# Kernel optimization log

Hardware: AMD Instinct MI355X
Metric: run time of the kernel (lower is better)

The kernel has to match this reference:

```python
import jax, jax.numpy as jnp
import numpy as np

B = 32768
IN_DIM, OUT_DIM, VAR_DIM = 2, 3, 50
KER_DIMS = [1024, 1024, 1024, 1024]
NSTEPS = 32  # fixed-step RK4 stand-in for adaptive odeint over t in [0, 1]


def setup_inputs() -> dict:
    key = jax.random.key(0)
    ks = jax.random.split(key, 11)
    x = jax.random.normal(ks[0], (B, IN_DIM), dtype=jnp.float32)
    dims = [VAR_DIM] + KER_DIMS + [VAR_DIM]
    inp = {"x": x}
    for i, (d1, d2) in enumerate(zip(dims[:-1], dims[1:])):
        # torch Linear(d1+1, d2): weight (d2, d1+1); stored here as (d1+1, d2)
        bound = 1.0 / np.sqrt(d1 + 1)
        inp[f"W{i}"] = jax.random.uniform(ks[1 + 2 * i], (d1 + 1, d2), jnp.float32, -bound, bound)
        inp[f"b{i}"] = jax.random.uniform(ks[2 + 2 * i], (d2,), jnp.float32, -bound, bound)
    return inp


def _odefunc(t, y, Ws, bs):
    # Each layer: concat time column, Linear, ReLU (except last) -- matches ODEfunc.forward
    out = y
    n = len(Ws)
    for i in range(n):
        tcol = jnp.full((out.shape[0], 1), t, dtype=out.dtype)
        h = jnp.concatenate([out, tcol], axis=1)
        out = h @ Ws[i] + bs[i]
        if i < n - 1:
            out = jax.nn.relu(out)
    return out


def _integrate(x, Ws, bs):
    # Pad input into var_dim state: out[:, :in_dim] = x, rest zeros
    y0 = jnp.zeros((x.shape[0], VAR_DIM), dtype=x.dtype).at[:, : x.shape[1]].set(x)
    dt = jnp.asarray(1.0 / NSTEPS, dtype=x.dtype)
    ts = jnp.arange(NSTEPS, dtype=x.dtype) * dt

    def step(y, t):
        k1 = _odefunc(t, y, Ws, bs)
        k2 = _odefunc(t + dt * 0.5, y + dt * 0.5 * k1, Ws, bs)
        k3 = _odefunc(t + dt * 0.5, y + dt * 0.5 * k2, Ws, bs)
        k4 = _odefunc(t + dt, y + dt * k3, Ws, bs)
        return y + (dt / 6.0) * (k1 + 2.0 * k2 + 2.0 * k3 + k4), None

    y1, _ = jax.lax.scan(step, y0, ts)
    return y1[:, :OUT_DIM]


def reference(x, W0, b0, W1, b1, W2, b2, W3, b3, W4, b4):
    Ws = (W0, W1, W2, W3, W4)
    bs = (b0, b1, b2, b3, b4)
    return _integrate(x, Ws, bs)
```

## Files before the change

### kernel.cpp

```cpp
#include <hip/hip_runtime.h>
#include <hip/hip_bf16.h>
#include <stdint.h>


typedef __bf16 bf16_t;
typedef bf16_t bf16x8 __attribute__((ext_vector_type(8)));
typedef float  f32x4  __attribute__((ext_vector_type(4)));

#define DEVI static __device__ __forceinline__

DEVI void gload_lds16(const bf16_t* gsrc, bf16_t* ldst) {
  __builtin_amdgcn_global_load_lds(
      (const __attribute__((address_space(1))) uint32_t*)gsrc,
      (__attribute__((address_space(3))) uint32_t*)ldst,
      16, 0, 0);
}

template<int K>
__global__ __launch_bounds__(512, 2) void gemm256(
    const bf16_t* __restrict__ A,
    const bf16_t* __restrict__ BT,
    const float* __restrict__ bias,
    const float* __restrict__ wtime,
    float t,
    bf16_t* __restrict__ C, int ldc,
    int M, int N)
{
  constexpr int NT = K / 64;
  static_assert(NT >= 2, "need >=2 K-tiles");

  __shared__ __align__(16) bf16_t As[2][256][64];
  __shared__ __align__(16) bf16_t Bs[2][256][64];

  const int tid  = threadIdx.x;
  const int wave = tid >> 6;
  const int lane = tid & 63;
  const int wr = wave >> 2;
  const int wc = wave & 3;

  int wg = blockIdx.x;
  {
    const int cpx = gridDim.x >> 3;
    wg = (wg & 7) * cpx + (wg >> 3);
  }
  const int nbn = N >> 8;
  const int bm = (wg / nbn) << 8;
  const int bn = (wg % nbn) << 8;

  const int srow = lane >> 3;
  const int scol = ((lane & 7) << 3) ^ ((lane & 32) >> 1) ^ ((wave & 1) << 5);
  const bf16_t* aS = A  + (size_t)(bm + wave * 8 + srow) * K + scol;
  const bf16_t* bS = BT + (size_t)(bn + wave * 8 + srow) * K + scol;
  bf16_t* aD = &As[0][0][0] + wave * 8 * 64;
  bf16_t* bD = &Bs[0][0][0] + wave * 8 * 64;

  auto stageHalf = [&](int kt, int isB, int h) {
    const int buf = kt & 1;
    const bf16_t* src = (isB ? bS : aS) + (size_t)(h * 128) * K + kt * 64;
    bf16_t*       dst = (isB ? bD : aD) + (buf * 256 + h * 128) * 64;
    gload_lds16(src,                  dst);
    gload_lds16(src + (size_t)64 * K, dst + 64 * 64);
  };
  auto stageTile = [&](int kt) {
    stageHalf(kt, 0, 0); stageHalf(kt, 0, 1);
    stageHalf(kt, 1, 0); stageHalf(kt, 1, 1);
  };

  const int fr = lane & 15;
  const int fq = lane >> 4;
  const int rsw = ((fr & 4) << 3) ^ ((fr & 8) << 3);

  bf16x8 ah0[8], ah1[8];
  bf16x8 bh0[4], bh1[4];
  f32x4  acc[8][4] = {};

  auto lda_into = [&](bf16x8 (&dst)[8], int buf, int mh) {
    const char* base = (const char*)&As[buf][0][0];
#pragma unroll
    for (int m = 0; m < 4; ++m)
#pragma unroll
      for (int kk = 0; kk < 2; ++kk) {
        int r  = wr * 128 + (mh * 4 + m) * 16 + fr;
        int cb = (kk * 64 + fq * 16) ^ rsw;
        dst[m * 2 + kk] = *(const bf16x8*)(base + r * 128 + cb);
      }
  };
  auto ldb_into = [&](bf16x8 (&dst)[4], int buf, int nh) {
    const char* base = (const char*)&Bs[buf][0][0];
#pragma unroll
    for (int n = 0; n < 2; ++n)
#pragma unroll
      for (int kk = 0; kk < 2; ++kk) {
        int r  = wc * 64 + (nh * 2 + n) * 16 + fr;
        int cb = (kk * 64 + fq * 16) ^ rsw;
        dst[n * 2 + kk] = *(const bf16x8*)(base + r * 128 + cb);
      }
  };
  auto mma_quad = [&](bf16x8 (&a)[8], bf16x8 (&b)[4], int mh, int nh) {
    __builtin_amdgcn_s_setprio(1);
#pragma unroll
    for (int m = 0; m < 4; ++m)
#pragma unroll
      for (int n = 0; n < 2; ++n)
#pragma unroll
        for (int kk = 0; kk < 2; ++kk)
          acc[mh * 4 + m][nh * 2 + n] = __builtin_amdgcn_mfma_f32_16x16x32_bf16(
              a[m * 2 + kk], b[n * 2 + kk],
              acc[mh * 4 + m][nh * 2 + n], 0, 0, 0);
    __builtin_amdgcn_s_setprio(0);
  };

  stageTile(0);
  asm volatile("s_waitcnt vmcnt(0)" ::: "memory");
  __builtin_amdgcn_s_barrier();
  lda_into(ah0, 0, 0);
  ldb_into(bh0, 0, 0);

  for (int t2 = 0; t2 < NT; ++t2) {
    const int buf = t2 & 1;
    if (t2 + 1 < NT) stageTile(t2 + 1);
    ldb_into(bh1, buf, 1);
    mma_quad(ah0, bh0, 0, 0);
    lda_into(ah1, buf, 1);
    mma_quad(ah0, bh1, 0, 1);
    mma_quad(ah1, bh0, 1, 0);
    if (t2 + 1 < NT) {
      asm volatile("s_waitcnt vmcnt(0)" ::: "memory");
      __builtin_amdgcn_s_barrier();
      lda_into(ah0, buf ^ 1, 0);
      ldb_into(bh0, buf ^ 1, 0);
    }
    mma_quad(ah1, bh1, 1, 1);
  }

#pragma unroll
  for (int n = 0; n < 4; ++n) {
    const int gcol = bn + wc * 64 + n * 16 + fr;
    const float bv = bias[gcol] + t * wtime[gcol];
#pragma unroll
    for (int m = 0; m < 8; ++m) {
      const int grow0 = bm + wr * 128 + m * 16 + (fq << 2);
#pragma unroll
      for (int r = 0; r < 4; ++r) {
        float v = acc[m][n][r] + bv;
        v = v > 0.0f ? v : 0.0f;
        C[(size_t)(grow0 + r) * ldc + gcol] = (bf16_t)v;
      }
    }
  }
}

template<int BM, int BN, int BK, int WROWS, int WCOLS, bool RELU, bool OUT_BF16>
__global__ __launch_bounds__(256) void gemm_bt(
    const bf16_t* __restrict__ A, int lda,
    const bf16_t* __restrict__ BT,
    const float* __restrict__ bias,
    const float* __restrict__ wtime,
    float t,
    void* __restrict__ Cv, int ldc,
    int M, int K)
{
  static_assert(BK == 64, "swizzle assumes BK=64");
  constexpr int MR  = BM / WROWS / 16;
  constexpr int NR  = BN / WCOLS / 16;
  constexpr int TPR = BK / 8;
  constexpr int RPW = 64 / TPR;
  constexpr int RPL = 4 * RPW;
  static_assert(BM % RPL == 0 && BN % RPL == 0, "tile staging mismatch");

  __shared__ bf16_t As[BM][BK];
  __shared__ bf16_t Bs[BN][BK];

  const int tid  = threadIdx.x;
  const int wave = tid >> 6;
  const int lane = tid & 63;
  const int wr = wave / WCOLS;
  const int wc = wave % WCOLS;
  const int bm = blockIdx.x * BM;
  const int bn = blockIdx.y * BN;
  const int lrow = lane >> 3;
  const int lcol = (((lane & 7) << 3) ^ ((lane & 32) >> 1) ^ ((wave & 1) << 5));

  const int fr = lane & 15;
  const int fq = lane >> 4;
  const int esw = ((fr & 4) << 2) ^ ((fr & 8) << 2);

  f32x4 acc[MR][NR] = {};

  for (int k0 = 0; k0 < K; k0 += BK) {
#pragma unroll
    for (int i = 0; i < BM / RPL; ++i) {
      const int rb = i * RPL + wave * RPW;
      gload_lds16(&A[(size_t)(bm + rb + lrow) * lda + k0 + lcol], &As[rb][0]);
    }
#pragma unroll
    for (int i = 0; i < BN / RPL; ++i) {
      const int rb = i * RPL + wave * RPW;
      gload_lds16(&BT[(size_t)(bn + rb + lrow) * K + k0 + lcol], &Bs[rb][0]);
    }
    __syncthreads();
#pragma unroll
    for (int kk = 0; kk < BK / 32; ++kk) {
      bf16x8 af[MR], bfr[NR];
      const int ecol = (kk * 32 + fq * 8) ^ esw;
#pragma unroll
      for (int m = 0; m < MR; ++m)
        af[m] = *(const bf16x8*)&As[wr * (BM / WROWS) + m * 16 + fr][ecol];
#pragma unroll
      for (int n = 0; n < NR; ++n)
        bfr[n] = *(const bf16x8*)&Bs[wc * (BN / WCOLS) + n * 16 + fr][ecol];
#pragma unroll
      for (int m = 0; m < MR; ++m)
#pragma unroll
        for (int n = 0; n < NR; ++n)
          acc[m][n] = __builtin_amdgcn_mfma_f32_16x16x32_bf16(
              af[m], bfr[n], acc[m][n], 0, 0, 0);
    }
    __syncthreads();
  }

#pragma unroll
  for (int n = 0; n < NR; ++n) {
    const int gcol = bn + wc * (BN / WCOLS) + n * 16 + fr;
    const float bv = bias[gcol] + t * wtime[gcol];
#pragma unroll
    for (int m = 0; m < MR; ++m) {
      const int grow0 = bm + wr * (BM / WROWS) + m * 16 + (fq << 2);
#pragma unroll
      for (int r = 0; r < 4; ++r) {
        float v = acc[m][n][r] + bv;
        if (RELU) v = v > 0.0f ? v : 0.0f;
        if constexpr (OUT_BF16)
          ((bf16_t*)Cv)[(size_t)(grow0 + r) * ldc + gcol] = (bf16_t)v;
        else
          ((float*)Cv)[(size_t)(grow0 + r) * ldc + gcol] = v;
      }
    }
  }
}

__global__ __launch_bounds__(256) void gemm_l4_rk4(
    const bf16_t* __restrict__ A, int lda,
    const bf16_t* __restrict__ BT,
    const float* __restrict__ bias,
    const float* __restrict__ wtime,
    float t,
    float* __restrict__ y, float* __restrict__ accb,
    bf16_t* __restrict__ ybf,
    float ca, float cs, int mode,
    int M, int K)
{
  constexpr int BM = 64, BN = 64, BK = 64;
  constexpr int MR = 2, NR = 2;

  __shared__ bf16_t As[BM][BK];
  __shared__ bf16_t Bs[BN][BK];

  const int tid  = threadIdx.x;
  const int wave = tid >> 6;
  const int lane = tid & 63;
  const int wr = wave >> 1;
  const int wc = wave & 1;
  const int bm = blockIdx.x * BM;
  const int lrow = lane >> 3;
  const int lcol = (((lane & 7) << 3) ^ ((lane & 32) >> 1) ^ ((wave & 1) << 5));

  const int fr = lane & 15;
  const int fq = lane >> 4;
  const int esw = ((fr & 4) << 2) ^ ((fr & 8) << 2);

  f32x4 acc[MR][NR] = {};

  for (int k0 = 0; k0 < K; k0 += BK) {
#pragma unroll
    for (int i = 0; i < 2; ++i) {
      const int rb = i * 32 + wave * 8;
      gload_lds16(&A[(size_t)(bm + rb + lrow) * lda + k0 + lcol], &As[rb][0]);
    }
#pragma unroll
    for (int i = 0; i < 2; ++i) {
      const int rb = i * 32 + wave * 8;
      gload_lds16(&BT[(size_t)(rb + lrow) * K + k0 + lcol], &Bs[rb][0]);
    }
    __syncthreads();
#pragma unroll
    for (int kk = 0; kk < 2; ++kk) {
      bf16x8 af[MR], bfr[NR];
      const int ecol = (kk * 32 + fq * 8) ^ esw;
#pragma unroll
      for (int m = 0; m < MR; ++m)
        af[m] = *(const bf16x8*)&As[wr * 32 + m * 16 + fr][ecol];
#pragma unroll
      for (int n = 0; n < NR; ++n)
        bfr[n] = *(const bf16x8*)&Bs[wc * 32 + n * 16 + fr][ecol];
#pragma unroll
      for (int m = 0; m < MR; ++m)
#pragma unroll
        for (int n = 0; n < NR; ++n)
          acc[m][n] = __builtin_amdgcn_mfma_f32_16x16x32_bf16(
              af[m], bfr[n], acc[m][n], 0, 0, 0);
    }
    __syncthreads();
  }

#pragma unroll
  for (int n = 0; n < NR; ++n) {
    const int gcol = wc * 32 + n * 16 + fr;
    const float bv = bias[gcol] + t * wtime[gcol];
#pragma unroll
    for (int m = 0; m < MR; ++m) {
      const int grow0 = bm + wr * 32 + m * 16 + (fq << 2);
#pragma unroll
      for (int r = 0; r < 4; ++r) {
        const float kv = acc[m][n][r] + bv;
        const size_t o = (size_t)(grow0 + r) * 64 + gcol;
        if (mode == 0) {
          accb[o] = kv;
          ybf[o] = (bf16_t)(y[o] + cs * kv);
        } else if (mode == 1) {
          accb[o] += ca * kv;
          ybf[o] = (bf16_t)(y[o] + cs * kv);
        } else {
          const float ny = y[o] + cs * (accb[o] + kv);
          y[o] = ny;
          ybf[o] = (bf16_t)ny;
        }
      }
    }
  }
}

__global__ void prep_weight(const float* __restrict__ W, const float* __restrict__ b,
                            bf16_t* __restrict__ WT, float* __restrict__ bias,
                            float* __restrict__ wtime,
                            int K, int N, int Kpad, int Npad)
{
  int idx = blockIdx.x * 256 + threadIdx.x;
  int total = Npad * Kpad;
  if (idx < total) {
    int n = idx / Kpad, k = idx % Kpad;
    float v = (n < N && k < K) ? W[(size_t)k * N + n] : 0.0f;
    WT[idx] = (bf16_t)v;
  }
  if (idx < Npad) {
    bias[idx]  = (idx < N) ? b[idx] : 0.0f;
    wtime[idx] = (idx < N) ? W[(size_t)K * N + idx] : 0.0f;
  }
}

__global__ void init_y(const float* __restrict__ x, float* __restrict__ y,
                       bf16_t* __restrict__ ybf, int M)
{
  int i = blockIdx.x * 256 + threadIdx.x;
  if (i < M * 64) {
    int m = i >> 6, c = i & 63;
    float v = (c < 2) ? x[m * 2 + c] : 0.0f;
    y[i] = v;
    ybf[i] = (bf16_t)v;
  }
}

__global__ void extract_out(const float* __restrict__ y, float* __restrict__ out, int M)
{
  int i = blockIdx.x * 256 + threadIdx.x;
  if (i < M * 3) {
    int m = i / 3, c = i % 3;
    out[i] = y[(size_t)m * 64 + c];
  }
}

extern "C" void kernel_launch(void* const* d_in, const int* in_sizes, int n_in,
                              void* d_out, int out_size, void* d_ws, size_t ws_size,
                              hipStream_t stream)
{
  (void)in_sizes; (void)n_in; (void)out_size; (void)ws_size;
  const int M = 32768;

  const float* x = (const float*)d_in[0];
  const float* Wp[5]; const float* bp[5];
  for (int i = 0; i < 5; ++i) {
    Wp[i] = (const float*)d_in[1 + 2 * i];
    bp[i] = (const float*)d_in[2 + 2 * i];
  }

  char* ws = (char*)d_ws; size_t off = 0;
  auto alloc = [&](size_t bytes) -> char* {
    char* p = ws + off; off += (bytes + 255) & ~(size_t)255; return p;
  };

  bf16_t* WT[5];
  WT[0] = (bf16_t*)alloc((size_t)1024 * 64 * 2);
  WT[1] = (bf16_t*)alloc((size_t)1024 * 1024 * 2);
  WT[2] = (bf16_t*)alloc((size_t)1024 * 1024 * 2);
  WT[3] = (bf16_t*)alloc((size_t)1024 * 1024 * 2);
  WT[4] = (bf16_t*)alloc((size_t)64 * 1024 * 2);
  float* bias[5]; float* wtm[5];
  for (int i = 0; i < 5; ++i) {
    int Np = (i == 4) ? 64 : 1024;
    bias[i] = (float*)alloc((size_t)Np * 4);
    wtm[i]  = (float*)alloc((size_t)Np * 4);
  }
  float*  y    = (float*)alloc((size_t)M * 64 * 4);
  float*  accb = (float*)alloc((size_t)M * 64 * 4);
  bf16_t* ybf  = (bf16_t*)alloc((size_t)M * 64 * 2);
  bf16_t* act0 = (bf16_t*)alloc((size_t)M * 1024 * 2);
  bf16_t* act1 = (bf16_t*)alloc((size_t)M * 1024 * 2);

  const int Kd[5]  = {50, 1024, 1024, 1024, 1024};
  const int Nd[5]  = {1024, 1024, 1024, 1024, 50};
  const int Kpd[5] = {64, 1024, 1024, 1024, 1024};
  const int Npd[5] = {1024, 1024, 1024, 1024, 64};
  for (int i = 0; i < 5; ++i) {
    int tot = Npd[i] * Kpd[i];
    prep_weight<<<dim3((tot + 255) / 256), 256, 0, stream>>>(
        Wp[i], bp[i], WT[i], bias[i], wtm[i], Kd[i], Nd[i], Kpd[i], Npd[i]);
  }

  init_y<<<dim3((M * 64 + 255) / 256), 256, 0, stream>>>(x, y, ybf, M);

  const float dtv = 1.0f / 32.0f;
  dim3 gL0(M / 128, 1024 / 128);
  dim3 g256(M / 256 * (1024 / 256));
  dim3 gL4(M / 64);

  auto run_net = [&](float t, float ca, float cs, int mode) {
    gemm_bt<128,128,64,2,2,true,true><<<gL0, 256, 0, stream>>>(
        ybf, 64, WT[0], bias[0], wtm[0], t, act0, 1024, M, 64);
    gemm256<1024><<<g256, 512, 0, stream>>>(
        act0, WT[1], bias[1], wtm[1], t, act1, 1024, M, 1024);
    gemm256<1024><<<g256, 512, 0, stream>>>(
        act1, WT[2], bias[2], wtm[2], t, act0, 1024, M, 1024);
    gemm256<1024><<<g256, 512, 0, stream>>>(
        act0, WT[3], bias[3], wtm[3], t, act1, 1024, M, 1024);
    gemm_l4_rk4<<<gL4, 256, 0, stream>>>(
        act1, 1024, WT[4], bias[4], wtm[4], t,
        y, accb, ybf, ca, cs, mode, M, 1024);
  };

  for (int i = 0; i < 32; ++i) {
    const float t0 = i * dtv;
    const float tm = t0 + 0.5f * dtv;
    const float t1 = t0 + dtv;
    run_net(t0, 0.0f, 0.5f * dtv, 0);
    run_net(tm, 2.0f, 0.5f * dtv, 1);
    run_net(tm, 2.0f, dtv,        1);
    run_net(t1, 0.0f, dtv / 6.0f, 2);
  }

  extract_out<<<dim3((M * 3 + 255) / 256), 256, 0, stream>>>(y, (float*)d_out, M);
}
```

Measured before the change: 35.17 ms.

## Use 4-wave 256x256 GEMM blocks with 128x128 per-wave tiles

The 1024x1024 hidden-layer GEMM kernel moves from 8 waves (2x4, 128x64 per wave) to 4 waves (2x2, 128x128 per wave) per 256x256 block. Each wave now holds 64 accumulator tiles, loads full 8-fragment A/B sets per k-substep and stages 16 LDS loads per tile. The aim is more MFMA work per LDS fragment read and fewer waves contending for LDS bandwidth. The cost is much higher register pressure and occupancy limited to one block per CU, which reduces latency hiding and risks spills.

```diff
diff --git a/kernel.cpp b/kernel.cpp
--- a/kernel.cpp
+++ b/kernel.cpp
@@ -17,7 +17,7 @@
 }
 
 template<int K>
-__global__ __launch_bounds__(512, 2) void gemm256(
+__global__ __launch_bounds__(256, 1) void gemm256(
     const bf16_t* __restrict__ A,
     const bf16_t* __restrict__ BT,
     const float* __restrict__ bias,
@@ -35,8 +35,8 @@
   const int tid  = threadIdx.x;
   const int wave = tid >> 6;
   const int lane = tid & 63;
-  const int wr = wave >> 2;
-  const int wc = wave & 3;
+  const int wr = wave >> 1;
+  const int wc = wave & 1;
 
   int wg = blockIdx.x;
   {
@@ -54,88 +54,77 @@
   bf16_t* aD = &As[0][0][0] + wave * 8 * 64;
   bf16_t* bD = &Bs[0][0][0] + wave * 8 * 64;
 
-  auto stageHalf = [&](int kt, int isB, int h) {
+  auto stageTile = [&](int kt) {
     const int buf = kt & 1;
-    const bf16_t* src = (isB ? bS : aS) + (size_t)(h * 128) * K + kt * 64;
-    bf16_t*       dst = (isB ? bD : aD) + (buf * 256 + h * 128) * 64;
-    gload_lds16(src,                  dst);
-    gload_lds16(src + (size_t)64 * K, dst + 64 * 64);
-  };
-  auto stageTile = [&](int kt) {
-    stageHalf(kt, 0, 0); stageHalf(kt, 0, 1);
-    stageHalf(kt, 1, 0); stageHalf(kt, 1, 1);
+#pragma unroll
+    for (int i = 0; i < 8; ++i) {
+      gload_lds16(aS + (size_t)(i * 32) * K + kt * 64, aD + (buf * 256 + i * 32) * 64);
+      gload_lds16(bS + (size_t)(i * 32) * K + kt * 64, bD + (buf * 256 + i * 32) * 64);
+    }
   };
 
   const int fr = lane & 15;
   const int fq = lane >> 4;
   const int rsw = ((fr & 4) << 3) ^ ((fr & 8) << 3);
 
-  bf16x8 ah0[8], ah1[8];
-  bf16x8 bh0[4], bh1[4];
-  f32x4  acc[8][4] = {};
-
-  auto lda_into = [&](bf16x8 (&dst)[8], int buf, int mh) {
+  bf16x8 a0[8], a1[8];
+  bf16x8 b0[8], b1[8];
+  f32x4  acc[8][8] = {};
+
+  auto lda_kk = [&](bf16x8 (&dst)[8], int buf, int kk) {
     const char* base = (const char*)&As[buf][0][0];
 #pragma unroll
-    for (int m = 0; m < 4; ++m)
-#pragma unroll
-      for (int kk = 0; kk < 2; ++kk) {
-        int r  = wr * 128 + (mh * 4 + m) * 16 + fr;
-        int cb = (kk * 64 + fq * 16) ^ rsw;
-        dst[m * 2 + kk] = *(const bf16x8*)(base + r * 128 + cb);
-      }
-  };
-  auto ldb_into = [&](bf16x8 (&dst)[4], int buf, int nh) {
+    for (int m = 0; m < 8; ++m) {
+      int r  = wr * 128 + m * 16 + fr;
+      int cb = (kk * 64 + fq * 16) ^ rsw;
+      dst[m] = *(const bf16x8*)(base + r * 128 + cb);
+    }
+  };
+  auto ldb_kk = [&](bf16x8 (&dst)[8], int buf, int kk) {
     const char* base = (const char*)&Bs[buf][0][0];
 #pragma unroll
-    for (int n = 0; n < 2; ++n)
-#pragma unroll
-      for (int kk = 0; kk < 2; ++kk) {
-        int r  = wc * 64 + (nh * 2 + n) * 16 + fr;
-        int cb = (kk * 64 + fq * 16) ^ rsw;
-        dst[n * 2 + kk] = *(const bf16x8*)(base + r * 128 + cb);
-      }
-  };
-  auto mma_quad = [&](bf16x8 (&a)[8], bf16x8 (&b)[4], int mh, int nh) {
+    for (int n = 0; n < 8; ++n) {
+      int r  = wc * 128 + n * 16 + fr;
+      int cb = (kk * 64 + fq * 16) ^ rsw;
+      dst[n] = *(const bf16x8*)(base + r * 128 + cb);
+    }
+  };
+  auto mma_all = [&](bf16x8 (&a)[8], bf16x8 (&b)[8]) {
     __builtin_amdgcn_s_setprio(1);
 #pragma unroll
-    for (int m = 0; m < 4; ++m)
-#pragma unroll
-      for (int n = 0; n < 2; ++n)
-#pragma unroll
-        for (int kk = 0; kk < 2; ++kk)
-          acc[mh * 4 + m][nh * 2 + n] = __builtin_amdgcn_mfma_f32_16x16x32_bf16(
-              a[m * 2 + kk], b[n * 2 + kk],
-              acc[mh * 4 + m][nh * 2 + n], 0, 0, 0);
+    for (int m = 0; m < 8; ++m)
+#pragma unroll
+      for (int n = 0; n < 8; ++n)
+        acc[m][n] = __builtin_amdgcn_mfma_f32_16x16x32_bf16(
+            a[m], b[n], acc[m][n], 0, 0, 0);
     __builtin_amdgcn_s_setprio(0);
   };
 
   stageTile(0);
   asm volatile("s_waitcnt vmcnt(0)" ::: "memory");
   __builtin_amdgcn_s_barrier();
-  lda_into(ah0, 0, 0);
-  ldb_into(bh0, 0, 0);
+  lda_kk(a0, 0, 0);
+  ldb_kk(b0, 0, 0);
 
   for (int t2 = 0; t2 < NT; ++t2) {
     const int buf = t2 & 1;
     if (t2 + 1 < NT) stageTile(t2 + 1);
-    ldb_into(bh1, buf, 1);
-    mma_quad(ah0, bh0, 0, 0);
-    lda_into(ah1, buf, 1);
-    mma_quad(ah0, bh1, 0, 1);
-    mma_quad(ah1, bh0, 1, 0);
+    lda_kk(a1, buf, 1);
+    ldb_kk(b1, buf, 1);
+    mma_all(a0, b0);
     if (t2 + 1 < NT) {
+      asm volatile("s_waitcnt lgkmcnt(0)" ::: "memory");
       asm volatile("s_waitcnt vmcnt(0)" ::: "memory");
       __builtin_amdgcn_s_barrier();
-      lda_into(ah0, buf ^ 1, 0);
-      ldb_into(bh0, buf ^ 1, 0);
-    }
-    mma_quad(ah1, bh1, 1, 1);
-  }
-
-#pragma unroll
-  for (int n = 0; n < 4; ++n) {
-    const int gcol = bn + wc * 64 + n * 16 + fr;
+      lda_kk(a0, buf ^ 1, 0);
+      ldb_kk(b0, buf ^ 1, 0);
+    }
+    mma_all(a1, b1);
+  }
+
+#pragma unroll
+  for (int n = 0; n < 8; ++n) {
+    const int gcol = bn + wc * 128 + n * 16 + fr;
     const float bv = bias[gcol] + t * wtime[gcol];
 #pragma unroll
     for (int m = 0; m < 8; ++m) {
@@ -426,11 +415,11 @@
   auto run_net = [&](float t, float ca, float cs, int mode) {
     gemm_bt<128,128,64,2,2,true,true><<<gL0, 256, 0, stream>>>(
         ybf, 64, WT[0], bias[0], wtm[0], t, act0, 1024, M, 64);
-    gemm256<1024><<<g256, 512, 0, stream>>>(
+    gemm256<1024><<<g256, 256, 0, stream>>>(
         act0, WT[1], bias[1], wtm[1], t, act1, 1024, M, 1024);
-    gemm256<1024><<<g256, 512, 0, stream>>>(
+    gemm256<1024><<<g256, 256, 0, stream>>>(
         act1, WT[2], bias[2], wtm[2], t, act0, 1024, M, 1024);
-    gemm256<1024><<<g256, 512, 0, stream>>>(
+    gemm256<1024><<<g256, 256, 0, stream>>>(
         act0, WT[3], bias[3], wtm[3], t, act1, 1024, M, 1024);
     gemm_l4_rk4<<<gL4, 256, 0, stream>>>(
         act1, 1024, WT[4], bias[4], wtm[4], t,
```

Measured after the change: 38.50 ms. 1.09x slower.

## Load B fragments directly from global into registers, drop B LDS staging

Applied to the files above, without the earlier changes.

B-operand tiles are no longer staged through shared memory. Each wave now reads its B fragments straight from global memory into registers, and the vmcnt waits are adjusted to overlap these loads with the MFMAs. This halves LDS use and removes the LDS writes and reads for B, which could allow more occupancy and less LDS traffic. In exchange, B rows are loaded redundantly across waves with less coalesced global accesses. The vmcnt counting is delicate: bh1 is loaded after the last mma, and the ordering of the waits relative to the A staging must be correct.

```diff
diff --git a/kernel.cpp b/kernel.cpp
--- a/kernel.cpp
+++ b/kernel.cpp
@@ -27,10 +27,9 @@
     int M, int N)
 {
   constexpr int NT = K / 64;
-  static_assert(NT >= 2, "need >=2 K-tiles");
+  static_assert(NT >= 3, "pipeline needs >=3 K-tiles");
 
   __shared__ __align__(16) bf16_t As[2][256][64];
-  __shared__ __align__(16) bf16_t Bs[2][256][64];
 
   const int tid  = threadIdx.x;
   const int wave = tid >> 6;
@@ -49,21 +48,18 @@
 
   const int srow = lane >> 3;
   const int scol = ((lane & 7) << 3) ^ ((lane & 32) >> 1) ^ ((wave & 1) << 5);
-  const bf16_t* aS = A  + (size_t)(bm + wave * 8 + srow) * K + scol;
-  const bf16_t* bS = BT + (size_t)(bn + wave * 8 + srow) * K + scol;
+  const bf16_t* aS = A + (size_t)(bm + wave * 8 + srow) * K + scol;
   bf16_t* aD = &As[0][0][0] + wave * 8 * 64;
-  bf16_t* bD = &Bs[0][0][0] + wave * 8 * 64;
-
-  auto stageHalf = [&](int kt, int isB, int h) {
+
+  auto stageTile = [&](int kt) {
     const int buf = kt & 1;
-    const bf16_t* src = (isB ? bS : aS) + (size_t)(h * 128) * K + kt * 64;
-    bf16_t*       dst = (isB ? bD : aD) + (buf * 256 + h * 128) * 64;
-    gload_lds16(src,                  dst);
-    gload_lds16(src + (size_t)64 * K, dst + 64 * 64);
-  };
-  auto stageTile = [&](int kt) {
-    stageHalf(kt, 0, 0); stageHalf(kt, 0, 1);
-    stageHalf(kt, 1, 0); stageHalf(kt, 1, 1);
+#pragma unroll
+    for (int h = 0; h < 2; ++h) {
+      const bf16_t* src = aS + (size_t)(h * 128) * K + kt * 64;
+      bf16_t*       dst = aD + (buf * 256 + h * 128) * 64;
+      gload_lds16(src,                  dst);
+      gload_lds16(src + (size_t)64 * K, dst + 64 * 64);
+    }
   };
 
   const int fr = lane & 15;
@@ -85,15 +81,14 @@
         dst[m * 2 + kk] = *(const bf16x8*)(base + r * 128 + cb);
       }
   };
-  auto ldb_into = [&](bf16x8 (&dst)[4], int buf, int nh) {
-    const char* base = (const char*)&Bs[buf][0][0];
+  auto ldbg = [&](bf16x8 (&dst)[4], int kt, int nh) {
 #pragma unroll
     for (int n = 0; n < 2; ++n)
 #pragma unroll
       for (int kk = 0; kk < 2; ++kk) {
-        int r  = wc * 64 + (nh * 2 + n) * 16 + fr;
-        int cb = (kk * 64 + fq * 16) ^ rsw;
-        dst[n * 2 + kk] = *(const bf16x8*)(base + r * 128 + cb);
+        const bf16_t* p = BT + (size_t)(bn + wc * 64 + nh * 32 + n * 16 + fr) * K
+                             + kt * 64 + kk * 32 + fq * 8;
+        dst[n * 2 + kk] = *(const bf16x8*)p;
       }
   };
   auto mma_quad = [&](bf16x8 (&a)[8], bf16x8 (&b)[4], int mh, int nh) {
@@ -111,26 +106,27 @@
   };
 
   stageTile(0);
-  asm volatile("s_waitcnt vmcnt(0)" ::: "memory");
+  ldbg(bh0, 0, 0);
+  ldbg(bh1, 0, 1);
+  asm volatile("s_waitcnt vmcnt(8)" ::: "memory");
   __builtin_amdgcn_s_barrier();
   lda_into(ah0, 0, 0);
-  ldb_into(bh0, 0, 0);
 
   for (int t2 = 0; t2 < NT; ++t2) {
     const int buf = t2 & 1;
     if (t2 + 1 < NT) stageTile(t2 + 1);
-    ldb_into(bh1, buf, 1);
+    lda_into(ah1, buf, 1);
     mma_quad(ah0, bh0, 0, 0);
-    lda_into(ah1, buf, 1);
     mma_quad(ah0, bh1, 0, 1);
     mma_quad(ah1, bh0, 1, 0);
     if (t2 + 1 < NT) {
-      asm volatile("s_waitcnt vmcnt(0)" ::: "memory");
+      ldbg(bh0, t2 + 1, 0);
+      asm volatile("s_waitcnt vmcnt(4)" ::: "memory");
       __builtin_amdgcn_s_barrier();
       lda_into(ah0, buf ^ 1, 0);
-      ldb_into(bh0, buf ^ 1, 0);
     }
     mma_quad(ah1, bh1, 1, 1);
+    if (t2 + 1 < NT) ldbg(bh1, t2 + 1, 1);
   }
 
 #pragma unroll
```

Result: slower. 41.45 ms (+17.9%).

## Fuse next evaluation's first layer into the last-layer RK4 update kernel

Applied to the files above, without the earlier changes.

The final-layer GEMM with the RK4 state update now also computes the next network evaluation's first layer (K=64 to 1024). It stages the new bf16 state tile in LDS and writes the ReLU activations straight to act0. This removes one kernel launch per evaluation and the global round-trip of the bf16 state buffer. In exchange the fused kernel does more work per block with only M/64 blocks and heavier register use, and the first layer is computed once up front outside the loop. The last iteration computes one unused layer-0 output.

```diff
diff --git a/kernel.cpp b/kernel.cpp
--- a/kernel.cpp
+++ b/kernel.cpp
@@ -239,14 +239,18 @@
   }
 }
 
-__global__ __launch_bounds__(256) void gemm_l4_rk4(
+__global__ __launch_bounds__(256) void gemm_l4_rk4_l0(
     const bf16_t* __restrict__ A, int lda,
     const bf16_t* __restrict__ BT,
     const float* __restrict__ bias,
     const float* __restrict__ wtime,
     float t,
+    const bf16_t* __restrict__ BT0,
+    const float* __restrict__ bias0,
+    const float* __restrict__ wtime0,
+    float tn,
     float* __restrict__ y, float* __restrict__ accb,
-    bf16_t* __restrict__ ybf,
+    bf16_t* __restrict__ act0,
     float ca, float cs, int mode,
     int M, int K)
 {
@@ -255,6 +259,7 @@
 
   __shared__ bf16_t As[BM][BK];
   __shared__ bf16_t Bs[BN][BK];
+  __shared__ bf16_t Ys[64][72];
 
   const int tid  = threadIdx.x;
   const int wave = tid >> 6;
@@ -309,21 +314,74 @@
     const float bv = bias[gcol] + t * wtime[gcol];
 #pragma unroll
     for (int m = 0; m < MR; ++m) {
-      const int grow0 = bm + wr * 32 + m * 16 + (fq << 2);
+      const int lr0 = wr * 32 + m * 16 + (fq << 2);
 #pragma unroll
       for (int r = 0; r < 4; ++r) {
         const float kv = acc[m][n][r] + bv;
-        const size_t o = (size_t)(grow0 + r) * 64 + gcol;
+        const size_t o = (size_t)(bm + lr0 + r) * 64 + gcol;
+        float yb;
         if (mode == 0) {
           accb[o] = kv;
-          ybf[o] = (bf16_t)(y[o] + cs * kv);
+          yb = y[o] + cs * kv;
         } else if (mode == 1) {
           accb[o] += ca * kv;
-          ybf[o] = (bf16_t)(y[o] + cs * kv);
+          yb = y[o] + cs * kv;
         } else {
           const float ny = y[o] + cs * (accb[o] + kv);
           y[o] = ny;
-          ybf[o] = (bf16_t)ny;
+          yb = ny;
+        }
+        Ys[lr0 + r][gcol] = (bf16_t)yb;
+      }
+    }
+  }
+  __syncthreads();
+
+  const int colbase = wave * 256;
+  bf16x8 af0[4][2];
+#pragma unroll
+  for (int m2 = 0; m2 < 4; ++m2)
+#pragma unroll
+    for (int kk = 0; kk < 2; ++kk)
+      af0[m2][kk] = *(const bf16x8*)&Ys[m2 * 16 + fr][kk * 32 + fq * 8];
+
+  bf16x8 bfA[4][2], bfB[4][2];
+  auto ldb0 = [&](bf16x8 (&d)[4][2], int g) {
+#pragma unroll
+    for (int n = 0; n < 4; ++n)
+#pragma unroll
+      for (int kk = 0; kk < 2; ++kk)
+        d[n][kk] = *(const bf16x8*)(BT0
+            + (size_t)(colbase + g * 64 + n * 16 + fr) * 64 + kk * 32 + fq * 8);
+  };
+  ldb0(bfA, 0);
+
+#pragma unroll
+  for (int g = 0; g < 4; ++g) {
+    bf16x8 (&bcur)[4][2]  = (g & 1) ? bfB : bfA;
+    bf16x8 (&bnext)[4][2] = (g & 1) ? bfA : bfB;
+    if (g + 1 < 4) ldb0(bnext, g + 1);
+    f32x4 acc2[4][4] = {};
+#pragma unroll
+    for (int kk = 0; kk < 2; ++kk)
+#pragma unroll
+      for (int m2 = 0; m2 < 4; ++m2)
+#pragma unroll
+        for (int n = 0; n < 4; ++n)
+          acc2[m2][n] = __builtin_amdgcn_mfma_f32_16x16x32_bf16(
+              af0[m2][kk], bcur[n][kk], acc2[m2][n], 0, 0, 0);
+#pragma unroll
+    for (int n = 0; n < 4; ++n) {
+      const int col = colbase + g * 64 + n * 16 + fr;
+      const float bv = bias0[col] + tn * wtime0[col];
+#pragma unroll
+      for (int m2 = 0; m2 < 4; ++m2) {
+        const int row0 = bm + m2 * 16 + (fq << 2);
+#pragma unroll
+        for (int r = 0; r < 4; ++r) {
+          float v = acc2[m2][n][r] + bv;
+          v = v > 0.0f ? v : 0.0f;
+          act0[(size_t)(row0 + r) * 1024 + col] = (bf16_t)v;
         }
       }
     }
@@ -423,28 +481,31 @@
   dim3 g256(M / 256 * (1024 / 256));
   dim3 gL4(M / 64);
 
-  auto run_net = [&](float t, float ca, float cs, int mode) {
-    gemm_bt<128,128,64,2,2,true,true><<<gL0, 256, 0, stream>>>(
-        ybf, 64, WT[0], bias[0], wtm[0], t, act0, 1024, M, 64);
+  gemm_bt<128,128,64,2,2,true,true><<<gL0, 256, 0, stream>>>(
+      ybf, 64, WT[0], bias[0], wtm[0], 0.0f, act0, 1024, M, 64);
+
+  auto run_eval = [&](float t, float tn, float ca, float cs, int mode) {
     gemm256<1024><<<g256, 512, 0, stream>>>(
         act0, WT[1], bias[1], wtm[1], t, act1, 1024, M, 1024);
     gemm256<1024><<<g256, 512, 0, stream>>>(
         act1, WT[2], bias[2], wtm[2], t, act0, 1024, M, 1024);
     gemm256<1024><<<g256, 512, 0, stream>>>(
         act0, WT[3], bias[3], wtm[3], t, act1, 1024, M, 1024);
-    gemm_l4_rk4<<<gL4, 256, 0, stream>>>(
+    gemm_l4_rk4_l0<<<gL4, 256, 0, stream>>>(
         act1, 1024, WT[4], bias[4], wtm[4], t,
-        y, accb, ybf, ca, cs, mode, M, 1024);
+        WT[0], bias[0], wtm[0], tn,
+        y, accb, act0, ca, cs, mode, M, 1024);
   };
 
   for (int i = 0; i < 32; ++i) {
     const float t0 = i * dtv;
     const float tm = t0 + 0.5f * dtv;
     const float t1 = t0 + dtv;
-    run_net(t0, 0.0f, 0.5f * dtv, 0);
-    run_net(tm, 2.0f, 0.5f * dtv, 1);
-    run_net(tm, 2.0f, dtv,        1);
-    run_net(t1, 0.0f, dtv / 6.0f, 2);
+    const float t0n = (i + 1) * dtv;
+    run_eval(t0, tm,  0.0f, 0.5f * dtv, 0);
+    run_eval(tm, tm,  2.0f, 0.5f * dtv, 1);
+    run_eval(tm, t1,  2.0f, dtv,        1);
+    run_eval(t1, t0n, 0.0f, dtv / 6.0f, 2);
   }
 
   extract_out<<<dim3((M * 3 + 255) / 256), 256, 0, stream>>>(y, (float*)d_out, M);
```

After: 33.69 ms. -4.2%, faster.
